# Performance work log

Measured on AMD Instinct MI355X. Metric: run time of the kernel, lower is better.

Reference implementation:

```python
import jax, jax.numpy as jnp
import numpy as np

HEADS = 16
DIM = 1024
HEAD_DIM = DIM // HEADS


def setup_inputs() -> dict:
    key = jax.random.key(0)
    k1, k2 = jax.random.split(key)
    images = jax.random.normal(k1, (2, 2048, DIM), dtype=jnp.float32)
    # torch nn.Linear(dim, 3*dim, bias=False): y = x @ W.T, W: [3*dim, dim].
    # Store as [dim, 3*dim] for direct x @ W_qkv.
    W_qkv = jax.random.normal(k2, (DIM, 3 * DIM), dtype=jnp.float32) / np.sqrt(DIM)
    return {"images": images, "W_qkv": W_qkv}


def reference(images, W_qkv):
    B, S, D = images.shape
    qkv = images @ W_qkv  # [B, S, 3D]
    q, k, v = jnp.split(qkv, 3, axis=-1)
    # [B, S, H, Dh] -> [B, H, S, Dh]
    def to_heads(t):
        return t.reshape(B, S, HEADS, HEAD_DIM).transpose(0, 2, 1, 3)
    q, k, v = to_heads(q), to_heads(k), to_heads(v)
    scale = 1.0 / jnp.sqrt(jnp.asarray(HEAD_DIM, dtype=q.dtype))
    scores = jnp.einsum('bhqd,bhkd->bhqk', q, k) * scale  # [B, H, S, S]
    probs = jax.nn.softmax(scores, axis=-1)
    out = jnp.einsum('bhqk,bhkd->bhqd', probs, v)  # [B, H, S, Dh]
    return out.transpose(0, 2, 1, 3).reshape(B, S, D)
```

## Files before the change

### kernel.cpp

```cpp
#include <hip/hip_runtime.h>
#include <hip/hip_bf16.h>
#include <math.h>

typedef __bf16 bf16x8 __attribute__((ext_vector_type(8)));
typedef float f32x4 __attribute__((ext_vector_type(4)));
typedef float f32x16 __attribute__((ext_vector_type(16)));
typedef unsigned short u16x8 __attribute__((ext_vector_type(8)));
typedef unsigned int u32x4 __attribute__((ext_vector_type(4)));
typedef unsigned short u16;

#define S_LEN 2048
#define DMODEL 1024
#define NH 16

__device__ __forceinline__ u16 f2bf(float f) {
    __bf16 b = (__bf16)f;
    return __builtin_bit_cast(u16, b);
}
__device__ __forceinline__ float bf2f(u16 u) {
    union { unsigned int i; float f; } v; v.i = ((unsigned int)u) << 16; return v.f;
}
__device__ __forceinline__ unsigned int pk2(float a, float b) {
    return (unsigned int)f2bf(a) | ((unsigned int)f2bf(b) << 16);
}

__device__ __forceinline__ void gload16(const u16* g, u16* lds_base) {
    __builtin_amdgcn_global_load_lds(
        (const __attribute__((address_space(1))) unsigned int*)g,
        (__attribute__((address_space(3))) unsigned int*)lds_base,
        16, 0, 0);
}

__global__ __launch_bounds__(256) void cvt_x(const float* __restrict__ in, u16* __restrict__ outp) {
    int i = (blockIdx.x * 256 + threadIdx.x) * 4;
    float4 v = *(const float4*)(in + i);
    outp[i + 0] = f2bf(v.x); outp[i + 1] = f2bf(v.y);
    outp[i + 2] = f2bf(v.z); outp[i + 3] = f2bf(v.w);
}

__global__ __launch_bounds__(256) void transpose_w(const float* __restrict__ W, u16* __restrict__ Wt) {
    __shared__ u16 tile[32][33];
    int n0 = blockIdx.x * 32, k0 = blockIdx.y * 32;
    int tx = threadIdx.x & 31, ty = threadIdx.x >> 5;
#pragma unroll
    for (int i = 0; i < 4; i++) {
        int k = ty + i * 8;
        tile[k][tx] = f2bf(W[(size_t)(k0 + k) * 3072 + n0 + tx]);
    }
    __syncthreads();
#pragma unroll
    for (int i = 0; i < 4; i++) {
        int n = ty + i * 8;
        Wt[(size_t)(n0 + n) * 1024 + k0 + tx] = tile[tx][n];
    }
}

__global__ __launch_bounds__(256) void qkv_gemm(const u16* __restrict__ A, const u16* __restrict__ Bt,
                                                u16* __restrict__ C) {
    __shared__ alignas(16) u16 As[128 * 64];
    __shared__ alignas(16) u16 Bs[128 * 64];
    const int tid = threadIdx.x, l = tid & 63, w = tid >> 6;
    const int bm = blockIdx.y, bn = blockIdx.x;
    const int wm = w >> 1, wn = w & 1;
    const int c0 = l & 15, g = l >> 4;
    f32x4 acc[4][4] = {};
    for (int kt = 0; kt < 1024; kt += 64) {
        __syncthreads();
#pragma unroll
        for (int n = 0; n < 4; n++) {
            int i = tid + n * 256;
            int r = i >> 3, c = i & 7;
            int cs = c ^ (r & 7);
            u16* dstA = As + (size_t)(w * 64 + n * 256) * 8;
            u16* dstB = Bs + (size_t)(w * 64 + n * 256) * 8;
            gload16(A + (size_t)(bm * 128 + r) * 1024 + kt + cs * 8, dstA);
            gload16(Bt + (size_t)(bn * 128 + r) * 1024 + kt + cs * 8, dstB);
        }
        __syncthreads();
#pragma unroll
        for (int kk = 0; kk < 2; kk++) {
            bf16x8 af[4], bfr[4];
#pragma unroll
            for (int m = 0; m < 4; m++) {
                int row = wm * 64 + m * 16 + c0;
                af[m] = *(const bf16x8*)((const char*)As + row * 128 + (((g + kk * 4) ^ (row & 7)) << 4));
            }
#pragma unroll
            for (int n = 0; n < 4; n++) {
                int row = wn * 64 + n * 16 + c0;
                bfr[n] = *(const bf16x8*)((const char*)Bs + row * 128 + (((g + kk * 4) ^ (row & 7)) << 4));
            }
#pragma unroll
            for (int m = 0; m < 4; m++)
#pragma unroll
                for (int n = 0; n < 4; n++)
                    acc[m][n] = __builtin_amdgcn_mfma_f32_16x16x32_bf16(af[m], bfr[n], acc[m][n], 0, 0, 0);
        }
    }
#pragma unroll
    for (int m = 0; m < 4; m++)
#pragma unroll
        for (int n = 0; n < 4; n++)
#pragma unroll
            for (int j = 0; j < 4; j++) {
                int row = bm * 128 + wm * 64 + m * 16 + 4 * g + j;
                int col = bn * 128 + wn * 64 + n * 16 + c0;
                C[(size_t)row * 3072 + col] = f2bf(acc[m][n][j]);
            }
}

__global__ __launch_bounds__(256) void transpose_v(const u16* __restrict__ QKV, u16* __restrict__ Vtp) {
    __shared__ u16 tile[64][72];
    const int bh = blockIdx.x >> 5, st = blockIdx.x & 31;
    const int b = bh >> 4, h = bh & 15;
    const u16* src = QKV + (size_t)b * S_LEN * 3072 + 2048 + h * 64;
    const int sl = threadIdx.x >> 2;
    const int cg = (threadIdx.x & 3) * 16;
#pragma unroll
    for (int ii = 0; ii < 2; ii++) {
        u16x8 v = *(const u16x8*)(src + (size_t)(st * 64 + sl) * 3072 + cg + ii * 8);
        *(u16x8*)&tile[sl][cg + ii * 8] = v;
    }
    __syncthreads();
    const int dl = threadIdx.x >> 2;
#pragma unroll
    for (int ii = 0; ii < 2; ii++) {
        u16x8 o;
#pragma unroll
        for (int q = 0; q < 8; q++) {
            int p = cg + ii * 8 + q;
            o[q] = tile[p][dl];
        }
        *(u16x8*)(Vtp + ((size_t)bh * 64 + dl) * S_LEN + st * 64 + cg + ii * 8) = o;
    }
}

__global__ __launch_bounds__(256, 2) void attn8(const u16* __restrict__ QKV, const u16* __restrict__ Vtp,
                                                float* __restrict__ outp) {
    __shared__ alignas(16) u16 Ks[2][64 * 64];
    __shared__ alignas(16) u16 Vs[2][64 * 64];
    const int bid = blockIdx.x;
    const int wg = ((bid & 7) << 6) | (bid >> 3);
    const int tid = threadIdx.x, l = tid & 63, w = tid >> 6;
    const int qt = wg & 15, bh = wg >> 4;
    const int b = bh >> 4, h = bh & 15;
    const int l5 = l & 31, hi = l >> 5;
    const u16* Qb = QKV + (size_t)b * S_LEN * 3072 + h * 64;
    const u16* Kb = Qb + 1024;
    const u16* Vb = Vtp + (size_t)bh * 64 * S_LEN;
    const int qbase = qt * 128 + w * 32;

    const int r0 = tid >> 3, cs0 = (tid & 7) ^ (r0 & 7);
    const int i1 = tid + 256, r1 = i1 >> 3, cs1 = (i1 & 7) ^ (r1 & 7);
    const int dbA = (w * 64) * 8, dbB = (256 + w * 64) * 8;

    int off[2][4];
#pragma unroll
    for (int x = 0; x < 2; x++)
#pragma unroll
        for (int ks = 0; ks < 4; ks++)
            off[x][ks] = (x * 32 + l5) * 128 + (((2 * ks + hi) ^ (l5 & 7)) << 4);

    bf16x8 qf[4];
    {
        const float qs = 0.125f * 1.44269504f;
#pragma unroll
        for (int ks = 0; ks < 4; ks++) {
            u16x8 v = *(const u16x8*)(Qb + (size_t)(qbase + l5) * 3072 + ks * 16 + hi * 8);
            bf16x8 q;
#pragma unroll
            for (int j = 0; j < 8; j++) q[j] = (__bf16)(bf2f(v[j]) * qs);
            qf[ks] = q;
        }
    }
    bf16x8 vone;
#pragma unroll
    for (int j = 0; j < 8; j++) vone[j] = (__bf16)1.0f;

    float m_r = -INFINITY;
    f32x16 accO0 = {}, accO1 = {}, accL = {};

    gload16(Kb + (size_t)r0 * 3072 + cs0 * 8, Ks[0] + dbA);
    gload16(Kb + (size_t)r1 * 3072 + cs1 * 8, Ks[0] + dbB);
    gload16(Vb + (size_t)r0 * S_LEN + cs0 * 8, Vs[0] + dbA);
    gload16(Vb + (size_t)r1 * S_LEN + cs1 * 8, Vs[0] + dbB);

    for (int t = 0; t < 32; t++) {
        const int cur = t & 1;
        __syncthreads();
        if (t + 1 < 32) {
            const int kvn = (t + 1) * 64;
            gload16(Kb + (size_t)(kvn + r0) * 3072 + cs0 * 8, Ks[cur ^ 1] + dbA);
            gload16(Kb + (size_t)(kvn + r1) * 3072 + cs1 * 8, Ks[cur ^ 1] + dbB);
            gload16(Vb + (size_t)r0 * S_LEN + kvn + cs0 * 8, Vs[cur ^ 1] + dbA);
            gload16(Vb + (size_t)r1 * S_LEN + kvn + cs1 * 8, Vs[cur ^ 1] + dbB);
        }
        const char* Kc = (const char*)Ks[cur];
        const char* Vc = (const char*)Vs[cur];
        f32x16 sck0 = {}, sck1 = {};
        __builtin_amdgcn_s_setprio(1);
#pragma unroll
        for (int ks = 0; ks < 4; ks++) {
            bf16x8 kf0 = *(const bf16x8*)(Kc + off[0][ks]);
            bf16x8 kf1 = *(const bf16x8*)(Kc + off[1][ks]);
            sck0 = __builtin_amdgcn_mfma_f32_32x32x16_bf16(kf0, qf[ks], sck0, 0, 0, 0);
            sck1 = __builtin_amdgcn_mfma_f32_32x32x16_bf16(kf1, qf[ks], sck1, 0, 0, 0);
        }
        __builtin_amdgcn_s_setprio(0);
        float mx;
        {
            float a0 = fmaxf(fmaxf(sck0[0], sck0[1]), sck0[2]);
            float a1 = fmaxf(fmaxf(sck0[3], sck0[4]), sck0[5]);
            float a2 = fmaxf(fmaxf(sck0[6], sck0[7]), sck0[8]);
            float a3 = fmaxf(fmaxf(sck0[9], sck0[10]), sck0[11]);
            float a4 = fmaxf(fmaxf(sck0[12], sck0[13]), sck0[14]);
            float a5 = fmaxf(fmaxf(sck0[15], sck1[0]), sck1[1]);
            float a6 = fmaxf(fmaxf(sck1[2], sck1[3]), sck1[4]);
            float a7 = fmaxf(fmaxf(sck1[5], sck1[6]), sck1[7]);
            float a8 = fmaxf(fmaxf(sck1[8], sck1[9]), sck1[10]);
            float a9 = fmaxf(fmaxf(sck1[11], sck1[12]), sck1[13]);
            float aa = fmaxf(sck1[14], sck1[15]);
            mx = fmaxf(fmaxf(fmaxf(fmaxf(a0, a1), fmaxf(a2, a3)), fmaxf(fmaxf(a4, a5), fmaxf(a6, a7))),
                       fmaxf(fmaxf(a8, a9), aa));
        }
        mx = fmaxf(mx, __shfl_xor(mx, 32));
        if (!__all(mx <= m_r + 8.f)) {
            float mnew = fmaxf(m_r, mx);
            float alpha = __builtin_amdgcn_exp2f(m_r - mnew);
            m_r = mnew;
#pragma unroll
            for (int r = 0; r < 16; r++) {
                int cr = (r & 3) + 8 * (r >> 2) + 4 * hi;
                float ar = __shfl(alpha, cr);
                accL[r] *= ar; accO0[r] *= ar; accO1[r] *= ar;
            }
        }
#pragma unroll
        for (int r = 0; r < 16; r++) {
            sck0[r] = __builtin_amdgcn_exp2f(sck0[r] - m_r);
            sck1[r] = __builtin_amdgcn_exp2f(sck1[r] - m_r);
        }
        unsigned int gA[2][2][2], gB[2][2][2], rcvE[2][2][2];
#pragma unroll
        for (int kb = 0; kb < 2; kb++) {
            const f32x16& s = kb ? sck1 : sck0;
#pragma unroll
            for (int t2 = 0; t2 < 2; t2++) {
                int ue = 8 * t2, uo = 8 * t2 + 4;
                gA[kb][t2][0] = pk2(s[ue + 0], s[ue + 1]);
                gA[kb][t2][1] = pk2(s[ue + 2], s[ue + 3]);
                gB[kb][t2][0] = pk2(s[uo + 0], s[uo + 1]);
                gB[kb][t2][1] = pk2(s[uo + 2], s[uo + 3]);
#pragma unroll
                for (int p = 0; p < 2; p++) {
                    unsigned int E = hi ? gA[kb][t2][p] : gB[kb][t2][p];
                    rcvE[kb][t2][p] = __shfl_xor((int)E, 32);
                }
            }
        }
        __builtin_amdgcn_s_setprio(1);
#pragma unroll
        for (int ks = 0; ks < 4; ks++) {
            const int kb = ks >> 1, t2 = ks & 1;
            u32x4 pu;
            pu[0] = hi ? rcvE[kb][t2][0] : gA[kb][t2][0];
            pu[1] = hi ? rcvE[kb][t2][1] : gA[kb][t2][1];
            pu[2] = hi ? gB[kb][t2][0] : rcvE[kb][t2][0];
            pu[3] = hi ? gB[kb][t2][1] : rcvE[kb][t2][1];
            bf16x8 pf = __builtin_bit_cast(bf16x8, pu);
            bf16x8 vf0 = *(const bf16x8*)(Vc + off[0][ks]);
            bf16x8 vf1 = *(const bf16x8*)(Vc + off[1][ks]);
            accL = __builtin_amdgcn_mfma_f32_32x32x16_bf16(pf, vone, accL, 0, 0, 0);
            accO0 = __builtin_amdgcn_mfma_f32_32x32x16_bf16(pf, vf0, accO0, 0, 0, 0);
            accO1 = __builtin_amdgcn_mfma_f32_32x32x16_bf16(pf, vf1, accO1, 0, 0, 0);
        }
        __builtin_amdgcn_s_setprio(0);
    }
#pragma unroll
    for (int r = 0; r < 16; r++) {
        int cr = (r & 3) + 8 * (r >> 2) + 4 * hi;
        float inv = 1.0f / accL[r];
        float* op = outp + ((size_t)b * S_LEN + qbase + cr) * DMODEL + h * 64;
        op[l5] = accO0[r] * inv;
        op[32 + l5] = accO1[r] * inv;
    }
}

extern "C" void kernel_launch(void* const* d_in, const int* in_sizes, int n_in,
                              void* d_out, int out_size, void* d_ws, size_t ws_size,
                              hipStream_t stream) {
    const float* X = (const float*)d_in[0];
    const float* W = (const float*)d_in[1];
    float* out = (float*)d_out;

    u16* Xb  = (u16*)d_ws;
    u16* Wt  = Xb + (size_t)4096 * 1024;
    u16* QKV = Wt + (size_t)3072 * 1024;
    u16* Vtp = QKV + (size_t)4096 * 3072;

    cvt_x<<<4096, 256, 0, stream>>>(X, Xb);
    transpose_w<<<dim3(96, 32), 256, 0, stream>>>(W, Wt);
    qkv_gemm<<<dim3(24, 32), 256, 0, stream>>>(Xb, Wt, QKV);
    transpose_v<<<1024, 256, 0, stream>>>(QKV, Vtp);
    attn8<<<512, 256, 0, stream>>>(QKV, Vtp, out);
}
```

Before: 116.7 us.

## Split attention KV range in two blocks and merge partial results

Splits each query tile's KV sequence into two halves processed by separate workgroups, doubling the grid from 512 to 1024 blocks so more CUs stay busy. Each half writes normalized output (fp32 into the final buffer or fp16 into a scratch buffer) plus its row max and sum, and a new merge kernel combines them with a log-sum-exp weighting. It also folds the max subtraction into the MFMA accumulator initialization, keeps a zero-based running max, and replaces the shuffle-based P repacking with v_permlane32_swap. The trade-offs are an extra kernel launch with its memory traffic, and fp16 rounding of the second half's partial output.

```diff
diff --git a/kernel.cpp b/kernel.cpp
--- a/kernel.cpp
+++ b/kernel.cpp
@@ -7,11 +7,13 @@
 typedef float f32x16 __attribute__((ext_vector_type(16)));
 typedef unsigned short u16x8 __attribute__((ext_vector_type(8)));
 typedef unsigned int u32x4 __attribute__((ext_vector_type(4)));
+typedef _Float16 h16x4 __attribute__((ext_vector_type(4)));
 typedef unsigned short u16;
 
 #define S_LEN 2048
 #define DMODEL 1024
 #define NH 16
+#define NROWS 65536
 
 __device__ __forceinline__ u16 f2bf(float f) {
     __bf16 b = (__bf16)f;
@@ -135,19 +137,22 @@
     }
 }
 
-__global__ __launch_bounds__(256, 2) void attn8(const u16* __restrict__ QKV, const u16* __restrict__ Vtp,
-                                                float* __restrict__ outp) {
+__global__ __launch_bounds__(256, 2) void attn10(const u16* __restrict__ QKV, const u16* __restrict__ Vtp,
+                                                 float* __restrict__ outp, _Float16* __restrict__ Op1,
+                                                 float* __restrict__ Mp, float* __restrict__ Lp) {
     __shared__ alignas(16) u16 Ks[2][64 * 64];
     __shared__ alignas(16) u16 Vs[2][64 * 64];
     const int bid = blockIdx.x;
-    const int wg = ((bid & 7) << 6) | (bid >> 3);
+    const int wg = ((bid & 7) << 7) | (bid >> 3);
     const int tid = threadIdx.x, l = tid & 63, w = tid >> 6;
-    const int qt = wg & 15, bh = wg >> 4;
+    const int bh = wg >> 5, rest = wg & 31;
+    const int qt = rest >> 1, hf = rest & 1;
     const int b = bh >> 4, h = bh & 15;
     const int l5 = l & 31, hi = l >> 5;
     const u16* Qb = QKV + (size_t)b * S_LEN * 3072 + h * 64;
     const u16* Kb = Qb + 1024;
     const u16* Vb = Vtp + (size_t)bh * 64 * S_LEN;
+    const int kv0 = hf * 1024;
     const int qbase = qt * 128 + w * 32;
 
     const int r0 = tid >> 3, cs0 = (tid & 7) ^ (r0 & 7);
@@ -177,19 +182,19 @@
 #pragma unroll
     for (int j = 0; j < 8; j++) vone[j] = (__bf16)1.0f;
 
-    float m_r = -INFINITY;
+    float m_r = 0.f;
     f32x16 accO0 = {}, accO1 = {}, accL = {};
 
-    gload16(Kb + (size_t)r0 * 3072 + cs0 * 8, Ks[0] + dbA);
-    gload16(Kb + (size_t)r1 * 3072 + cs1 * 8, Ks[0] + dbB);
-    gload16(Vb + (size_t)r0 * S_LEN + cs0 * 8, Vs[0] + dbA);
-    gload16(Vb + (size_t)r1 * S_LEN + cs1 * 8, Vs[0] + dbB);
-
-    for (int t = 0; t < 32; t++) {
+    gload16(Kb + (size_t)(kv0 + r0) * 3072 + cs0 * 8, Ks[0] + dbA);
+    gload16(Kb + (size_t)(kv0 + r1) * 3072 + cs1 * 8, Ks[0] + dbB);
+    gload16(Vb + (size_t)r0 * S_LEN + kv0 + cs0 * 8, Vs[0] + dbA);
+    gload16(Vb + (size_t)r1 * S_LEN + kv0 + cs1 * 8, Vs[0] + dbB);
+
+    for (int t = 0; t < 16; t++) {
         const int cur = t & 1;
         __syncthreads();
-        if (t + 1 < 32) {
-            const int kvn = (t + 1) * 64;
+        if (t + 1 < 16) {
+            const int kvn = kv0 + (t + 1) * 64;
             gload16(Kb + (size_t)(kvn + r0) * 3072 + cs0 * 8, Ks[cur ^ 1] + dbA);
             gload16(Kb + (size_t)(kvn + r1) * 3072 + cs1 * 8, Ks[cur ^ 1] + dbB);
             gload16(Vb + (size_t)r0 * S_LEN + kvn + cs0 * 8, Vs[cur ^ 1] + dbA);
@@ -197,7 +202,10 @@
         }
         const char* Kc = (const char*)Ks[cur];
         const char* Vc = (const char*)Vs[cur];
-        f32x16 sck0 = {}, sck1 = {};
+        f32x16 sck0, sck1;
+        const float nm = -m_r;
+#pragma unroll
+        for (int r = 0; r < 16; r++) { sck0[r] = nm; sck1[r] = nm; }
         __builtin_amdgcn_s_setprio(1);
 #pragma unroll
         for (int ks = 0; ks < 4; ks++) {
@@ -223,66 +231,102 @@
             mx = fmaxf(fmaxf(fmaxf(fmaxf(a0, a1), fmaxf(a2, a3)), fmaxf(fmaxf(a4, a5), fmaxf(a6, a7))),
                        fmaxf(fmaxf(a8, a9), aa));
         }
-        mx = fmaxf(mx, __shfl_xor(mx, 32));
-        if (!__all(mx <= m_r + 8.f)) {
-            float mnew = fmaxf(m_r, mx);
-            float alpha = __builtin_amdgcn_exp2f(m_r - mnew);
-            m_r = mnew;
+        if (!__all(mx <= 8.f)) {
+            float mxr = fmaxf(mx, __shfl_xor(mx, 32));
+            float adj = fmaxf(mxr, 0.f);
+            float alpha = __builtin_amdgcn_exp2f(-adj);
+            m_r += adj;
 #pragma unroll
             for (int r = 0; r < 16; r++) {
                 int cr = (r & 3) + 8 * (r >> 2) + 4 * hi;
                 float ar = __shfl(alpha, cr);
                 accL[r] *= ar; accO0[r] *= ar; accO1[r] *= ar;
             }
+#pragma unroll
+            for (int r = 0; r < 16; r++) { sck0[r] -= adj; sck1[r] -= adj; }
         }
 #pragma unroll
         for (int r = 0; r < 16; r++) {
-            sck0[r] = __builtin_amdgcn_exp2f(sck0[r] - m_r);
-            sck1[r] = __builtin_amdgcn_exp2f(sck1[r] - m_r);
-        }
-        unsigned int gA[2][2][2], gB[2][2][2], rcvE[2][2][2];
-#pragma unroll
-        for (int kb = 0; kb < 2; kb++) {
-            const f32x16& s = kb ? sck1 : sck0;
-#pragma unroll
-            for (int t2 = 0; t2 < 2; t2++) {
-                int ue = 8 * t2, uo = 8 * t2 + 4;
-                gA[kb][t2][0] = pk2(s[ue + 0], s[ue + 1]);
-                gA[kb][t2][1] = pk2(s[ue + 2], s[ue + 3]);
-                gB[kb][t2][0] = pk2(s[uo + 0], s[uo + 1]);
-                gB[kb][t2][1] = pk2(s[uo + 2], s[uo + 3]);
-#pragma unroll
-                for (int p = 0; p < 2; p++) {
-                    unsigned int E = hi ? gA[kb][t2][p] : gB[kb][t2][p];
-                    rcvE[kb][t2][p] = __shfl_xor((int)E, 32);
-                }
-            }
+            sck0[r] = __builtin_amdgcn_exp2f(sck0[r]);
+            sck1[r] = __builtin_amdgcn_exp2f(sck1[r]);
         }
         __builtin_amdgcn_s_setprio(1);
 #pragma unroll
         for (int ks = 0; ks < 4; ks++) {
-            const int kb = ks >> 1, t2 = ks & 1;
-            u32x4 pu;
-            pu[0] = hi ? rcvE[kb][t2][0] : gA[kb][t2][0];
-            pu[1] = hi ? rcvE[kb][t2][1] : gA[kb][t2][1];
-            pu[2] = hi ? gB[kb][t2][0] : rcvE[kb][t2][0];
-            pu[3] = hi ? gB[kb][t2][1] : rcvE[kb][t2][1];
+            const int t2 = ks & 1;
+            const f32x16& s = (ks & 2) ? sck1 : sck0;
+            const int ue = 8 * t2, uo = ue + 4;
+            unsigned int y0 = pk2(s[ue + 0], s[ue + 1]);
+            unsigned int y1 = pk2(s[ue + 2], s[ue + 3]);
+            unsigned int x0 = pk2(s[uo + 0], s[uo + 1]);
+            unsigned int x1 = pk2(s[uo + 2], s[uo + 3]);
+            asm("v_permlane32_swap_b32 %0, %1" : "+v"(y0), "+v"(x0));
+            asm("v_permlane32_swap_b32 %0, %1" : "+v"(y1), "+v"(x1));
+            u32x4 pu; pu[0] = y0; pu[1] = y1; pu[2] = x0; pu[3] = x1;
             bf16x8 pf = __builtin_bit_cast(bf16x8, pu);
             bf16x8 vf0 = *(const bf16x8*)(Vc + off[0][ks]);
             bf16x8 vf1 = *(const bf16x8*)(Vc + off[1][ks]);
-            accL = __builtin_amdgcn_mfma_f32_32x32x16_bf16(pf, vone, accL, 0, 0, 0);
+            accL  = __builtin_amdgcn_mfma_f32_32x32x16_bf16(pf, vone, accL, 0, 0, 0);
             accO0 = __builtin_amdgcn_mfma_f32_32x32x16_bf16(pf, vf0, accO0, 0, 0, 0);
             accO1 = __builtin_amdgcn_mfma_f32_32x32x16_bf16(pf, vf1, accO1, 0, 0, 0);
         }
         __builtin_amdgcn_s_setprio(0);
     }
-#pragma unroll
-    for (int r = 0; r < 16; r++) {
-        int cr = (r & 3) + 8 * (r >> 2) + 4 * hi;
-        float inv = 1.0f / accL[r];
-        float* op = outp + ((size_t)b * S_LEN + qbase + cr) * DMODEL + h * 64;
-        op[l5] = accO0[r] * inv;
-        op[32 + l5] = accO1[r] * inv;
+    const int rowg0 = bh * 2048 + qbase;
+    if (hf == 0) {
+#pragma unroll
+        for (int r = 0; r < 16; r++) {
+            int cr = (r & 3) + 8 * (r >> 2) + 4 * hi;
+            float inv = 1.0f / accL[r];
+            float* op = outp + ((size_t)b * S_LEN + qbase + cr) * DMODEL + h * 64;
+            op[l5] = accO0[r] * inv;
+            op[32 + l5] = accO1[r] * inv;
+        }
+    } else {
+#pragma unroll
+        for (int r = 0; r < 16; r++) {
+            int cr = (r & 3) + 8 * (r >> 2) + 4 * hi;
+            float inv = 1.0f / accL[r];
+            _Float16* op = Op1 + (size_t)(rowg0 + cr) * 64;
+            op[l5] = (_Float16)(accO0[r] * inv);
+            op[32 + l5] = (_Float16)(accO1[r] * inv);
+        }
+    }
+    if (hi == 0) Mp[hf * NROWS + rowg0 + l5] = m_r;
+    if (l5 == 0) {
+#pragma unroll
+        for (int r = 0; r < 16; r++) {
+            int cr = (r & 3) + 8 * (r >> 2) + 4 * hi;
+            Lp[hf * NROWS + rowg0 + cr] = accL[r];
+        }
+    }
+}
+
+__global__ __launch_bounds__(256) void attn_merge(float* __restrict__ outp, const _Float16* __restrict__ Op1,
+                                                  const float* __restrict__ Mp, const float* __restrict__ Lp) {
+    int t = blockIdx.x * 256 + threadIdx.x;
+    int r = t >> 2;
+    int dc = (t & 3) * 16;
+    int bh = r >> 11, srow = r & 2047;
+    int b = bh >> 4, h = bh & 15;
+    float m0 = Mp[r], m1 = Mp[NROWS + r];
+    float l0 = Lp[r], l1 = Lp[NROWS + r];
+    float M = fmaxf(m0, m1);
+    float w0 = __builtin_amdgcn_exp2f(m0 - M) * l0;
+    float w1 = __builtin_amdgcn_exp2f(m1 - M) * l1;
+    float inv = 1.0f / (w0 + w1);
+    float a0 = w0 * inv, a1 = w1 * inv;
+    float* op = outp + ((size_t)b * S_LEN + srow) * DMODEL + h * 64 + dc;
+    const _Float16* o1 = Op1 + (size_t)r * 64 + dc;
+#pragma unroll
+    for (int q = 0; q < 4; q++) {
+        float4 v0 = *(const float4*)(op + q * 4);
+        h16x4 v1 = *(const h16x4*)(o1 + q * 4);
+        v0.x = a0 * v0.x + a1 * (float)v1[0];
+        v0.y = a0 * v0.y + a1 * (float)v1[1];
+        v0.z = a0 * v0.z + a1 * (float)v1[2];
+        v0.w = a0 * v0.w + a1 * (float)v1[3];
+        *(float4*)(op + q * 4) = v0;
     }
 }
 
@@ -297,10 +341,14 @@
     u16* Wt  = Xb + (size_t)4096 * 1024;
     u16* QKV = Wt + (size_t)3072 * 1024;
     u16* Vtp = QKV + (size_t)4096 * 3072;
+    _Float16* Op1 = (_Float16*)Xb;
+    float* Mp = (float*)Wt;
+    float* Lp = Mp + 2 * NROWS;
 
     cvt_x<<<4096, 256, 0, stream>>>(X, Xb);
     transpose_w<<<dim3(96, 32), 256, 0, stream>>>(W, Wt);
     qkv_gemm<<<dim3(24, 32), 256, 0, stream>>>(Xb, Wt, QKV);
     transpose_v<<<1024, 256, 0, stream>>>(QKV, Vtp);
-    attn8<<<512, 256, 0, stream>>>(QKV, Vtp, out);
-}
+    attn10<<<1024, 256, 0, stream>>>(QKV, Vtp, out, Op1, Mp, Lp);
+    attn_merge<<<1024, 256, 0, stream>>>(out, Op1, Mp, Lp);
+}
```

New measurement: 123.6 us. 5.9% more time.
